# Optimization experiments

Hardware: AMD Instinct MI355X
Metric: run time of the kernel (lower is better)

## Reference

```python
import jax, jax.numpy as jnp
import numpy as np

DIM = 1024

def setup_inputs() -> dict:
    key = jax.random.key(0)
    k1, k2, k3, k4 = jax.random.split(key, 4)
    B, L, D = 32, 2048, DIM
    x = jax.random.normal(k1, (B, D), dtype=jnp.float32)
    context = jax.random.normal(k2, (B, L, D), dtype=jnp.float32)
    # linear_concatWa: Linear(2*dim, dim, bias=False) -> weight [dim, 2*dim]
    Wa = jax.random.normal(k3, (D, 2 * D), dtype=jnp.float32) * (1.0 / np.sqrt(2 * D))
    # linear_concatVa: Linear(dim, 1, bias=False) -> weight [1, dim]
    Va = jax.random.normal(k4, (1, D), dtype=jnp.float32) * (1.0 / np.sqrt(D))
    return {"x": x, "context": context, "Wa": Wa, "Va": Va}


def reference(x, context, Wa, Va):
    # concat-mode additive (Bahdanau) attention.
    # Wa @ cat(ht, hs) == ht @ Wa[:, :D].T + hs @ Wa[:, D:].T  (avoids materializing concat)
    D = x.shape[-1]
    Wa_t, Wa_s = Wa[:, :D], Wa[:, D:]              # each [D, D]
    ht_proj = jnp.einsum('bd,kd->bk', x, Wa_t)     # [B, D]
    hs_proj = jnp.einsum('bld,kd->blk', context, Wa_s)  # [B, L, D]
    hidden = jnp.tanh(ht_proj[:, None, :] + hs_proj)    # [B, L, D]
    scores = jnp.einsum('blk,ok->bl', hidden, Va)       # [B, L]  (Va: [1, D])
    attn = jax.nn.softmax(scores, axis=-1)               # [B, L]
    weighted = jnp.einsum('bl,bld->bd', attn, context)   # [B, D]
    return weighted, attn
```

## Files before the change

### kernel.cpp

```cpp
#include <hip/hip_runtime.h>
#include <hip/hip_bf16.h>
#include <cstdint>
#include <cstddef>

#define DIM 1024
#define B_SZ 32
#define L_SZ 2048

#define BM 128
#define BN 128

#define CVT_BLOCKS 8192
#define HT_BLOCKS  512
#define WA_BLOCKS  512

typedef __attribute__((ext_vector_type(8))) short bf16x8;
typedef __attribute__((ext_vector_type(4))) float floatx4;

static __device__ __forceinline__ unsigned cvt2_bf16_rne(float a, float b) {
    unsigned ua = __builtin_bit_cast(unsigned, a);
    unsigned ub = __builtin_bit_cast(unsigned, b);
    ua = (ua + 0x7FFFu + ((ua >> 16) & 1u)) >> 16;
    ub = (ub + 0x7FFFu + ((ub >> 16) & 1u)) >> 16;
    return ua | (ub << 16);
}

static __device__ __forceinline__ float bf2f(unsigned u16) {
    return __builtin_bit_cast(float, u16 << 16);
}

static __device__ __forceinline__ float tanh_fast(float x) {
    float e = __expf(2.0f * x);
    return 1.0f - 2.0f * __builtin_amdgcn_rcpf(e + 1.0f);
}

static __device__ __forceinline__ void gld_lds16(const void* g, void* lds) {
    __builtin_amdgcn_global_load_lds(
        (const __attribute__((address_space(1))) unsigned int*)g,
        (__attribute__((address_space(3))) unsigned int*)lds,
        16, 0, 0);
}

__global__ __launch_bounds__(256) void pre_kernel(
    const float* __restrict__ x, const float* __restrict__ ctx,
    const float* __restrict__ Wa,
    unsigned short* __restrict__ ctxB, unsigned short* __restrict__ WaB,
    float* __restrict__ ht, float* __restrict__ scores,
    float* __restrict__ weighted)
{
    const int bid = blockIdx.x, t = threadIdx.x;

    if (bid < CVT_BLOCKS) {
        const long n8 = (long)B_SZ * L_SZ * DIM / 8;
        const long stride = (long)CVT_BLOCKS * 256;
        for (long i = (long)bid * 256 + t; i < n8; i += stride) {
            const float4 a = ((const float4*)ctx)[i * 2];
            const float4 b = ((const float4*)ctx)[i * 2 + 1];
            uint4 o;
            o.x = cvt2_bf16_rne(a.x, a.y);
            o.y = cvt2_bf16_rne(a.z, a.w);
            o.z = cvt2_bf16_rne(b.x, b.y);
            o.w = cvt2_bf16_rne(b.z, b.w);
            ((uint4*)ctxB)[i] = o;
        }
    } else if (bid < CVT_BLOCKS + HT_BLOCKS) {
        const int lb = bid - CVT_BLOCKS;
        const int gi = lb * 256 + t;
        if (gi < B_SZ * L_SZ) scores[gi] = 0.f;
        const int b = lb >> 4, kb = lb & 15;
        __shared__ float xs[DIM];
        for (int i = t; i < DIM; i += 256) xs[i] = x[b * DIM + i];
        __syncthreads();
        const int wave = t >> 6, lane = t & 63;
        const float4* xs4 = (const float4*)xs;
        for (int kk = 0; kk < 16; ++kk) {
            const int k = kb * 64 + wave * 16 + kk;
            const float4* wr = (const float4*)(Wa + (size_t)k * (2 * DIM));
            float s = 0.f;
            #pragma unroll
            for (int d = 0; d < DIM / 4; d += 64) {
                const float4 w4 = wr[d + lane];
                const float4 x4 = xs4[d + lane];
                s += w4.x * x4.x + w4.y * x4.y + w4.z * x4.z + w4.w * x4.w;
            }
            #pragma unroll
            for (int off = 32; off > 0; off >>= 1) s += __shfl_xor(s, off);
            if (lane == 0) ht[b * DIM + k] = s;
        }
    } else {
        const int lb = bid - CVT_BLOCKS - HT_BLOCKS;
        const int i = lb * 256 + t;
        if (i < B_SZ * DIM) weighted[i] = 0.f;
        const int k = i >> 7, dc = i & 127;
        const float* s = Wa + (size_t)k * (2 * DIM) + DIM + dc * 8;
        const float4 a = ((const float4*)s)[0];
        const float4 b4 = ((const float4*)s)[1];
        uint4 o;
        o.x = cvt2_bf16_rne(a.x, a.y);
        o.y = cvt2_bf16_rne(a.z, a.w);
        o.z = cvt2_bf16_rne(b4.x, b4.y);
        o.w = cvt2_bf16_rne(b4.z, b4.w);
        ((uint4*)(WaB + (size_t)k * DIM + dc * 8))[0] = o;
    }
}

__global__ __launch_bounds__(256) void gemm_score_bf16(
    const unsigned short* __restrict__ A, const unsigned short* __restrict__ Bm,
    const float* __restrict__ Va, const float* __restrict__ ht,
    float* __restrict__ scores)
{
    __shared__ __align__(16) unsigned short As[BM * 64];
    __shared__ __align__(16) unsigned short Bs[BN * 64];
    const int t = threadIdx.x;
    const int n0 = blockIdx.x * BN;
    const int m0 = blockIdx.y * BM;
    const int lane = t & 63, wave = t >> 6;
    const int l15 = lane & 15, quad = lane >> 4;
    const int wm = (wave >> 1) * 64, wn = (wave & 1) * 64;

    const int lr = lane >> 3;
    const int lc = (lane & 7) ^ lr;
    const size_t aRow = (size_t)(m0 + wave * 32 + lr);
    const size_t bRow = (size_t)(n0 + wave * 32 + lr);

    floatx4 acc[4][4];
    #pragma unroll
    for (int i = 0; i < 4; ++i)
        #pragma unroll
        for (int j = 0; j < 4; ++j) acc[i][j] = (floatx4)0.f;

    for (int k0 = 0; k0 < DIM; k0 += 64) {
        #pragma unroll
        for (int q = 0; q < 4; ++q) {
            gld_lds16(A + (aRow + q * 8) * DIM + k0 + lc * 8,
                      &As[(wave * 32 + q * 8) * 64]);
            gld_lds16(Bm + (bRow + q * 8) * DIM + k0 + lc * 8,
                      &Bs[(wave * 32 + q * 8) * 64]);
        }
        __syncthreads();

        bf16x8 af[2][4], bv[2][4];
        #pragma unroll
        for (int kb = 0; kb < 2; ++kb) {
            #pragma unroll
            for (int i = 0; i < 4; ++i) {
                const int r = wm + i * 16 + l15;
                const int c = (kb * 4 + quad) ^ (r & 7);
                af[kb][i] = *(const bf16x8*)&As[r * 64 + c * 8];
            }
            #pragma unroll
            for (int j = 0; j < 4; ++j) {
                const int r = wn + j * 16 + l15;
                const int c = (kb * 4 + quad) ^ (r & 7);
                bv[kb][j] = *(const bf16x8*)&Bs[r * 64 + c * 8];
            }
        }
        #pragma unroll
        for (int kb = 0; kb < 2; ++kb)
            #pragma unroll
            for (int i = 0; i < 4; ++i)
                #pragma unroll
                for (int j = 0; j < 4; ++j)
                    acc[i][j] = __builtin_amdgcn_mfma_f32_16x16x32_bf16(
                        af[kb][i], bv[kb][j], acc[i][j], 0, 0, 0);
        __syncthreads();
    }

    const int bb = m0 >> 11;
    float htv[4], vav[4];
    #pragma unroll
    for (int j = 0; j < 4; ++j) {
        const int ng = n0 + wn + j * 16 + l15;
        htv[j] = ht[bb * DIM + ng];
        vav[j] = Va[ng];
    }
    #pragma unroll
    for (int i = 0; i < 4; ++i) {
        #pragma unroll
        for (int r = 0; r < 4; ++r) {
            float s = 0.f;
            #pragma unroll
            for (int j = 0; j < 4; ++j)
                s += tanh_fast(acc[i][j][r] + htv[j]) * vav[j];
            s += __shfl_xor(s, 8);
            s += __shfl_xor(s, 4);
            s += __shfl_xor(s, 2);
            s += __shfl_xor(s, 1);
            if (l15 == 0)
                atomicAdd(&scores[m0 + wm + i * 16 + quad * 4 + r], s);
        }
    }
}

__global__ __launch_bounds__(256) void post_kernel(
    const float* __restrict__ scores, const unsigned short* __restrict__ ctxB,
    float* __restrict__ attn, float* __restrict__ weighted)
{
    const int b = blockIdx.x, slice = blockIdx.y, t = threadIdx.x;
    const float* sc = scores + b * L_SZ;
    __shared__ float red[256];
    __shared__ float att[128];

    float m = -1e30f;
    for (int l = t; l < L_SZ; l += 256) m = fmaxf(m, sc[l]);
    red[t] = m; __syncthreads();
    for (int s = 128; s > 0; s >>= 1) { if (t < s) red[t] = fmaxf(red[t], red[t + s]); __syncthreads(); }
    m = red[0]; __syncthreads();
    float sum = 0.f;
    for (int l = t; l < L_SZ; l += 256) sum += __expf(sc[l] - m);
    red[t] = sum; __syncthreads();
    for (int s = 128; s > 0; s >>= 1) { if (t < s) red[t] += red[t + s]; __syncthreads(); }
    const float inv = 1.0f / red[0];

    const int l0 = slice * 128;
    if (t < 128) {
        const float av = __expf(sc[l0 + t] - m) * inv;
        att[t] = av;
        attn[b * L_SZ + l0 + t] = av;
    }
    __syncthreads();

    const unsigned short* cb = ctxB + ((size_t)b * L_SZ + l0) * DIM + t * 4;
    float a0 = 0.f, a1 = 0.f, a2 = 0.f, a3 = 0.f;
    for (int l = 0; l < 128; ++l) {
        const float a = att[l];
        const uint2 v = *(const uint2*)(cb + (size_t)l * DIM);
        a0 += a * bf2f(v.x & 0xFFFFu);
        a1 += a * bf2f(v.x >> 16);
        a2 += a * bf2f(v.y & 0xFFFFu);
        a3 += a * bf2f(v.y >> 16);
    }
    float* o = weighted + b * DIM + t * 4;
    atomicAdd(o + 0, a0);
    atomicAdd(o + 1, a1);
    atomicAdd(o + 2, a2);
    atomicAdd(o + 3, a3);
}

#define LDS_STRIDE 40
__global__ __launch_bounds__(256) void ht_kernel_fb(const float* __restrict__ x,
                                                    const float* __restrict__ Wa,
                                                    float* __restrict__ ht,
                                                    float* __restrict__ scores,
                                                    float* __restrict__ weighted) {
    const int b = blockIdx.x, kb = blockIdx.y, t = threadIdx.x;
    const int gidx = (b * 16 + kb) * 256 + t;
    if (gidx < B_SZ * L_SZ) scores[gidx] = 0.f;
    if (gidx < B_SZ * DIM) weighted[gidx] = 0.f;
    __shared__ float xs[DIM];
    for (int i = t; i < DIM; i += 256) xs[i] = x[b * DIM + i];
    __syncthreads();
    const int wave = t >> 6, lane = t & 63;
    for (int kk = 0; kk < 16; ++kk) {
        const int k = kb * 64 + wave * 16 + kk;
        const float* wr = Wa + (size_t)k * (2 * DIM);
        float s = 0.f;
        #pragma unroll
        for (int d = 0; d < DIM; d += 64) s += xs[d + lane] * wr[d + lane];
        #pragma unroll
        for (int off = 32; off > 0; off >>= 1) s += __shfl_xor(s, off);
        if (lane == 0) ht[b * DIM + k] = s;
    }
}

__global__ __launch_bounds__(256, 2) void gemm_score_kernel(
    const float* __restrict__ ctx, const float* __restrict__ Wa,
    const float* __restrict__ Va, const float* __restrict__ ht,
    float* __restrict__ scores)
{
    __shared__ unsigned short As[BM * LDS_STRIDE];
    __shared__ unsigned short Bs[BN * LDS_STRIDE];
    const int t = threadIdx.x;
    const int n0 = blockIdx.x * BN;
    const int m0 = blockIdx.y * BM;
    const int lane = t & 63, wave = t >> 6;
    const int l15 = lane & 15, quad = lane >> 4;
    const int wm = (wave >> 1) * 64, wn = (wave & 1) * 64;
    const int srow = t >> 3;
    const int scol = (t & 7) * 4;
    const float* aBase = ctx + (size_t)(m0 + srow) * DIM + scol;
    const float* bBase = Wa + (size_t)(n0 + srow) * (2 * DIM) + DIM + scol;

    floatx4 acc[4][4];
    #pragma unroll
    for (int i = 0; i < 4; ++i)
        #pragma unroll
        for (int j = 0; j < 4; ++j) acc[i][j] = (floatx4)0.f;

    for (int k0 = 0; k0 < DIM; k0 += 32) {
        __syncthreads();
        #pragma unroll
        for (int r = 0; r < 4; ++r) {
            const float4 va = *(const float4*)(aBase + (size_t)(r * 32) * DIM + k0);
            const float4 vb = *(const float4*)(bBase + (size_t)(r * 32) * (2 * DIM) + k0);
            *(uint2*)&As[(srow + r * 32) * LDS_STRIDE + scol] =
                make_uint2(cvt2_bf16_rne(va.x, va.y), cvt2_bf16_rne(va.z, va.w));
            *(uint2*)&Bs[(srow + r * 32) * LDS_STRIDE + scol] =
                make_uint2(cvt2_bf16_rne(vb.x, vb.y), cvt2_bf16_rne(vb.z, vb.w));
        }
        __syncthreads();
        bf16x8 af[4], bfr[4];
        #pragma unroll
        for (int i = 0; i < 4; ++i)
            af[i] = *(const bf16x8*)&As[(wm + i * 16 + l15) * LDS_STRIDE + quad * 8];
        #pragma unroll
        for (int j = 0; j < 4; ++j)
            bfr[j] = *(const bf16x8*)&Bs[(wn + j * 16 + l15) * LDS_STRIDE + quad * 8];
        #pragma unroll
        for (int i = 0; i < 4; ++i)
            #pragma unroll
            for (int j = 0; j < 4; ++j)
                acc[i][j] = __builtin_amdgcn_mfma_f32_16x16x32_bf16(af[i], bfr[j], acc[i][j], 0, 0, 0);
    }
    const int bb = m0 >> 11;
    float htv[4], vav[4];
    #pragma unroll
    for (int j = 0; j < 4; ++j) {
        const int ng = n0 + wn + j * 16 + l15;
        htv[j] = ht[bb * DIM + ng];
        vav[j] = Va[ng];
    }
    #pragma unroll
    for (int i = 0; i < 4; ++i) {
        #pragma unroll
        for (int r = 0; r < 4; ++r) {
            float s = 0.f;
            #pragma unroll
            for (int j = 0; j < 4; ++j)
                s += tanh_fast(acc[i][j][r] + htv[j]) * vav[j];
            s += __shfl_xor(s, 8);
            s += __shfl_xor(s, 4);
            s += __shfl_xor(s, 2);
            s += __shfl_xor(s, 1);
            if (l15 == 0)
                atomicAdd(&scores[m0 + wm + i * 16 + quad * 4 + r], s);
        }
    }
}

__global__ __launch_bounds__(256) void post_kernel_fb(
    const float* __restrict__ scores, const float* __restrict__ ctx,
    float* __restrict__ attn, float* __restrict__ weighted)
{
    const int b = blockIdx.x, slice = blockIdx.y, t = threadIdx.x;
    const float* sc = scores + b * L_SZ;
    __shared__ float red[256];
    __shared__ float att[128];
    float m = -1e30f;
    for (int l = t; l < L_SZ; l += 256) m = fmaxf(m, sc[l]);
    red[t] = m; __syncthreads();
    for (int s = 128; s > 0; s >>= 1) { if (t < s) red[t] = fmaxf(red[t], red[t + s]); __syncthreads(); }
    m = red[0]; __syncthreads();
    float sum = 0.f;
    for (int l = t; l < L_SZ; l += 256) sum += __expf(sc[l] - m);
    red[t] = sum; __syncthreads();
    for (int s = 128; s > 0; s >>= 1) { if (t < s) red[t] += red[t + s]; __syncthreads(); }
    const float inv = 1.0f / red[0];
    const int l0 = slice * 128;
    if (t < 128) {
        const float av = __expf(sc[l0 + t] - m) * inv;
        att[t] = av;
        attn[b * L_SZ + l0 + t] = av;
    }
    __syncthreads();
    const float* cb = ctx + ((size_t)b * L_SZ + l0) * DIM + t * 4;
    float4 w = make_float4(0.f, 0.f, 0.f, 0.f);
    for (int l = 0; l < 128; ++l) {
        const float a = att[l];
        const float4 c = *(const float4*)(cb + (size_t)l * DIM);
        w.x += a * c.x; w.y += a * c.y; w.z += a * c.z; w.w += a * c.w;
    }
    float* o = weighted + b * DIM + t * 4;
    atomicAdd(o + 0, w.x);
    atomicAdd(o + 1, w.y);
    atomicAdd(o + 2, w.z);
    atomicAdd(o + 3, w.w);
}

extern "C" void kernel_launch(void* const* d_in, const int* in_sizes, int n_in,
                              void* d_out, int out_size, void* d_ws, size_t ws_size,
                              hipStream_t stream) {
    const float* x   = (const float*)d_in[0];
    const float* ctx = (const float*)d_in[1];
    const float* Wa  = (const float*)d_in[2];
    const float* Va  = (const float*)d_in[3];

    float* out      = (float*)d_out;
    float* weighted = out;
    float* attn     = out + B_SZ * DIM;

    float* scores = (float*)d_ws;
    float* ht     = scores + B_SZ * L_SZ;

    const size_t base = (size_t)(B_SZ * L_SZ + B_SZ * DIM) * sizeof(float);
    const size_t need = base + (size_t)DIM * DIM * 2
                      + (size_t)B_SZ * L_SZ * DIM * 2;

    if (ws_size >= need) {
        unsigned short* WaB  = (unsigned short*)((char*)d_ws + base);
        unsigned short* ctxB = WaB + (size_t)DIM * DIM;
        pre_kernel<<<CVT_BLOCKS + HT_BLOCKS + WA_BLOCKS, 256, 0, stream>>>(
            x, ctx, Wa, ctxB, WaB, ht, scores, weighted);
        gemm_score_bf16<<<dim3(DIM / BN, (B_SZ * L_SZ) / BM), 256, 0, stream>>>(
            ctxB, WaB, Va, ht, scores);
        post_kernel<<<dim3(B_SZ, 16), 256, 0, stream>>>(scores, ctxB, attn, weighted);
    } else {
        ht_kernel_fb<<<dim3(B_SZ, 16), 256, 0, stream>>>(x, Wa, ht, scores, weighted);
        gemm_score_kernel<<<dim3(DIM / BN, (B_SZ * L_SZ) / BM), 256, 0, stream>>>(
            ctx, Wa, Va, ht, scores);
        post_kernel_fb<<<dim3(B_SZ, 16), 256, 0, stream>>>(scores, ctx, attn, weighted);
    }
}
```

Baseline: 601.2 us.

## Remap GEMM blocks across XCDs, split softmax stats, restructure bf16 conversion

The GEMM now runs on a 1D grid whose block index is permuted so that blocks landing on the same XCD (bid&7) work on nearby M tiles and share all N tiles, which should improve L2 reuse of A rows. The softmax max/sum reduction moves into a separate stats_kernel that runs once per batch, instead of being recomputed by each of the 16 slice blocks in post_kernel. The context conversion loop becomes a fixed four-iteration unrolled loop with coalesced float4 loads and uint2 stores. The price is an extra kernel launch and an extra round trip of attn through memory.

```diff
diff --git a/kernel.cpp b/kernel.cpp
--- a/kernel.cpp
+++ b/kernel.cpp
@@ -51,17 +51,15 @@
     const int bid = blockIdx.x, t = threadIdx.x;
 
     if (bid < CVT_BLOCKS) {
-        const long n8 = (long)B_SZ * L_SZ * DIM / 8;
-        const long stride = (long)CVT_BLOCKS * 256;
-        for (long i = (long)bid * 256 + t; i < n8; i += stride) {
-            const float4 a = ((const float4*)ctx)[i * 2];
-            const float4 b = ((const float4*)ctx)[i * 2 + 1];
-            uint4 o;
-            o.x = cvt2_bf16_rne(a.x, a.y);
-            o.y = cvt2_bf16_rne(a.z, a.w);
-            o.z = cvt2_bf16_rne(b.x, b.y);
-            o.w = cvt2_bf16_rne(b.z, b.w);
-            ((uint4*)ctxB)[i] = o;
+        const float4* c4 = (const float4*)ctx;
+        uint2* o2 = (uint2*)ctxB;
+        #pragma unroll
+        for (int it = 0; it < 4; ++it) {
+            const long g = ((long)it * CVT_BLOCKS + bid) * 512;
+            const float4 a = c4[g + t];
+            const float4 b = c4[g + 256 + t];
+            o2[g + t]       = make_uint2(cvt2_bf16_rne(a.x, a.y), cvt2_bf16_rne(a.z, a.w));
+            o2[g + 256 + t] = make_uint2(cvt2_bf16_rne(b.x, b.y), cvt2_bf16_rne(b.z, b.w));
         }
     } else if (bid < CVT_BLOCKS + HT_BLOCKS) {
         const int lb = bid - CVT_BLOCKS;
@@ -112,8 +110,12 @@
     __shared__ __align__(16) unsigned short As[BM * 64];
     __shared__ __align__(16) unsigned short Bs[BN * 64];
     const int t = threadIdx.x;
-    const int n0 = blockIdx.x * BN;
-    const int m0 = blockIdx.y * BM;
+
+    const int bid = blockIdx.x;
+    const int logical = (bid & 7) * 512 + (bid >> 3);
+    const int n0 = (logical & 7) * BN;
+    const int m0 = (logical >> 3) * BM;
+
     const int lane = t & 63, wave = t >> 6;
     const int l15 = lane & 15, quad = lane >> 4;
     const int wm = (wave >> 1) * 64, wn = (wave & 1) * 64;
@@ -192,14 +194,12 @@
     }
 }
 
-__global__ __launch_bounds__(256) void post_kernel(
-    const float* __restrict__ scores, const unsigned short* __restrict__ ctxB,
-    float* __restrict__ attn, float* __restrict__ weighted)
-{
-    const int b = blockIdx.x, slice = blockIdx.y, t = threadIdx.x;
+__global__ __launch_bounds__(256) void stats_kernel(
+    const float* __restrict__ scores, float* __restrict__ attn)
+{
+    const int b = blockIdx.x, t = threadIdx.x;
     const float* sc = scores + b * L_SZ;
     __shared__ float red[256];
-    __shared__ float att[128];
 
     float m = -1e30f;
     for (int l = t; l < L_SZ; l += 256) m = fmaxf(m, sc[l]);
@@ -212,16 +212,23 @@
     for (int s = 128; s > 0; s >>= 1) { if (t < s) red[t] += red[t + s]; __syncthreads(); }
     const float inv = 1.0f / red[0];
 
+    for (int l = t; l < L_SZ; l += 256)
+        attn[b * L_SZ + l] = __expf(sc[l] - m) * inv;
+}
+
+__global__ __launch_bounds__(256) void post_kernel(
+    const float* __restrict__ attn, const unsigned short* __restrict__ ctxB,
+    float* __restrict__ weighted)
+{
+    const int b = blockIdx.x, slice = blockIdx.y, t = threadIdx.x;
+    __shared__ float att[128];
     const int l0 = slice * 128;
-    if (t < 128) {
-        const float av = __expf(sc[l0 + t] - m) * inv;
-        att[t] = av;
-        attn[b * L_SZ + l0 + t] = av;
-    }
+    if (t < 128) att[t] = attn[b * L_SZ + l0 + t];
     __syncthreads();
 
     const unsigned short* cb = ctxB + ((size_t)b * L_SZ + l0) * DIM + t * 4;
     float a0 = 0.f, a1 = 0.f, a2 = 0.f, a3 = 0.f;
+    #pragma unroll 4
     for (int l = 0; l < 128; ++l) {
         const float a = att[l];
         const uint2 v = *(const uint2*)(cb + (size_t)l * DIM);
@@ -401,9 +408,10 @@
         unsigned short* ctxB = WaB + (size_t)DIM * DIM;
         pre_kernel<<<CVT_BLOCKS + HT_BLOCKS + WA_BLOCKS, 256, 0, stream>>>(
             x, ctx, Wa, ctxB, WaB, ht, scores, weighted);
-        gemm_score_bf16<<<dim3(DIM / BN, (B_SZ * L_SZ) / BM), 256, 0, stream>>>(
+        gemm_score_bf16<<<(DIM / BN) * ((B_SZ * L_SZ) / BM), 256, 0, stream>>>(
             ctxB, WaB, Va, ht, scores);
-        post_kernel<<<dim3(B_SZ, 16), 256, 0, stream>>>(scores, ctxB, attn, weighted);
+        stats_kernel<<<B_SZ, 256, 0, stream>>>(scores, attn);
+        post_kernel<<<dim3(B_SZ, 16), 256, 0, stream>>>(attn, ctxB, weighted);
     } else {
         ht_kernel_fb<<<dim3(B_SZ, 16), 256, 0, stream>>>(x, Wa, ht, scores, weighted);
         gemm_score_kernel<<<dim3(DIM / BN, (B_SZ * L_SZ) / BM), 256, 0, stream>>>(
```

After: 607.5 us. About the same (+1.1%).
